# Performance work log

Hardware: AMD Instinct MI355X
Metric: run time of the kernel (lower is better)

Reference implementation:

```python
import jax, jax.numpy as jnp
import numpy as np

IN_F = 1024
OUT_F = 4096
SEARCH_SPACE = [1, 2, 4, 8, 16]  # block sizes; powers of 2 dividing both dims, capped at 16


def circ_avg(W, bs):
    """Project W [out,in] onto block-circulant structure with block size bs.

    Equivalent to trans_to_cir_meng: within each (bs x bs) block, average each
    wrap-around diagonal and rebuild a circulant block C[k, j] = c[(k - j) % bs].
    """
    q, p = W.shape[0] // bs, W.shape[1] // bs
    t = W.reshape(q, bs, p, bs).transpose(0, 2, 1, 3)  # [q, p, bs, bs]
    i = jnp.arange(bs)
    # rot[..., i, j] = t[..., i, (i + j) % bs]  (rotate rows so diagonals align in columns)
    rot = t[:, :, i[:, None], (i[:, None] + i[None, :]) % bs]  # [q, p, bs, bs]
    c = rot.mean(axis=2)  # [q, p, bs]  mean over each diagonal
    # circulant block: w[..., k, j] = c[..., (k - j) % bs]
    w = c[:, :, (i[:, None] - i[None, :]) % bs]  # [q, p, bs, bs]
    return w.transpose(0, 2, 1, 3).reshape(W.shape)


def setup_inputs() -> dict:
    key = jax.random.key(0)
    k1, k2, k3, k4 = jax.random.split(key, 4)
    x = jax.random.normal(k1, (16, 512, IN_F), dtype=jnp.float32)
    weight = jax.random.normal(k2, (OUT_F, IN_F), dtype=jnp.float32) * 0.02
    alphas = jax.random.normal(k3, (len(SEARCH_SPACE),), dtype=jnp.float32)
    bias = jax.random.normal(k4, (OUT_F,), dtype=jnp.float32) * 0.02
    return {"x": x, "weight": weight, "alphas": alphas, "bias": bias}


def reference(x, weight, alphas, bias):
    # soft NAS mixture over block sizes (tau=1, soft mode)
    a = jax.nn.softmax(alphas)
    W = a[0] * weight  # block_size 1 == original weight
    for idx, bs in enumerate(SEARCH_SPACE[1:], start=1):
        W = W + a[idx] * circ_avg(weight, bs)
    # F.linear: y = x @ W^T + b
    return jnp.einsum("bsi,oi->bso", x, W) + bias
```

## Files before the change

kernel.cpp:

```cpp
#include <hip/hip_runtime.h>

typedef __bf16 bf16;
typedef __bf16 bf16x8 __attribute__((ext_vector_type(8)));
typedef float floatx4 __attribute__((ext_vector_type(4)));

#define IN_F  1024
#define OUT_F 4096
#define M_DIM 8192
#define K_DIM 1024
#define N_DIM 4096

__device__ __forceinline__ unsigned short f2bf(float f) {
    unsigned int u = __float_as_uint(f);
    u += 0x7FFFu + ((u >> 16) & 1u);
    return (unsigned short)(u >> 16);
}

__global__ __launch_bounds__(256) void build_w_kernel(
    const float* __restrict__ W, const float* __restrict__ alphas,
    unsigned short* __restrict__ Wb)
{
    __shared__ float Wl[16 * 256];

    const int t = threadIdx.x;
    const int rb = blockIdx.x >> 2;
    const int cb = blockIdx.x & 3;
    const int row0 = rb * 16, col0 = cb * 256;

    const float4* src = (const float4*)(W + (size_t)row0 * IN_F + col0);
    #pragma unroll
    for (int j = 0; j < 4; ++j) {
        const int idx = j * 256 + t;
        const int r = idx >> 6, c4 = idx & 63;
        ((float4*)Wl)[r * 64 + c4] = src[(size_t)r * 256 + c4];
    }

    float av[5];
    float mx = -1e30f;
    #pragma unroll
    for (int j = 0; j < 5; ++j) { av[j] = alphas[j]; mx = fmaxf(mx, av[j]); }
    float s = 0.f;
    #pragma unroll
    for (int j = 0; j < 5; ++j) { av[j] = __expf(av[j] - mx); s += av[j]; }
    const float inv = 1.f / s;
    #pragma unroll
    for (int j = 0; j < 5; ++j) av[j] *= inv;

    __syncthreads();

    const int k  = t >> 4;
    const int jj = t & 15;
    unsigned short ov[16];

    #pragma unroll
    for (int jb = 0; jb < 16; ++jb) {
        const int j = jb * 16 + jj;
        float acc = av[0] * Wl[k * 256 + j];
        #pragma unroll
        for (int e = 1; e <= 4; ++e) {
            const int bs   = 1 << e;
            const int mask = bs - 1;
            const int ol = k & ~mask;
            const int il = j & ~mask;
            const int d  = (k - j) & mask;
            float ssum = 0.f;
            #pragma unroll
            for (int r = 0; r < bs; ++r)
                ssum += Wl[(ol + r) * 256 + il + ((r + d) & mask)];
            acc += av[e] * (1.0f / (float)bs) * ssum;
        }
        ov[jb] = f2bf(acc);
    }

    __syncthreads();
    unsigned short* Wls = (unsigned short*)Wl;
    #pragma unroll
    for (int jb = 0; jb < 16; ++jb)
        Wls[k * 256 + jb * 16 + jj] = ov[jb];
    __syncthreads();

    const int kr = t >> 4, cg = t & 15;
    const uint4* p = (const uint4*)(Wls + kr * 256 + cg * 16);
    uint4* dst = (uint4*)(Wb + (size_t)(row0 + kr) * IN_F + col0 + cg * 16);
    dst[0] = p[0];
    dst[1] = p[1];
}

__global__ __launch_bounds__(256) void cvt_x_kernel(
    const float* __restrict__ x, uint4* __restrict__ xb)
{
    const int t = blockIdx.x * 256 + threadIdx.x;
    const float4* xv = (const float4*)x;
    const float4 v0 = xv[2 * t];
    const float4 v1 = xv[2 * t + 1];
    uint4 o;
    o.x = (unsigned)f2bf(v0.x) | ((unsigned)f2bf(v0.y) << 16);
    o.y = (unsigned)f2bf(v0.z) | ((unsigned)f2bf(v0.w) << 16);
    o.z = (unsigned)f2bf(v1.x) | ((unsigned)f2bf(v1.y) << 16);
    o.w = (unsigned)f2bf(v1.z) | ((unsigned)f2bf(v1.w) << 16);
    xb[t] = o;
}

__global__ __launch_bounds__(256) void gemm_bt_kernel(
    const bf16* __restrict__ A, const bf16* __restrict__ B,
    const float* __restrict__ bias, float* __restrict__ C)
{
    constexpr int N = N_DIM, K = K_DIM;
    constexpr int TM = 128, TN = 128, TK = 64;

    __shared__ __align__(16) bf16 As[TM * TK];
    __shared__ __align__(16) bf16 Bs[TN * TK];

    const int t    = threadIdx.x;
    const int w    = t >> 6;
    const int l    = t & 63;
    const int quad = l >> 4;
    const int l16  = l & 15;
    const int x7   = l16 & 7;

    const int nb = N / TN;
    const int bm = blockIdx.x / nb;
    const int bn = blockIdx.x % nb;

    const int wm = (w >> 1) * 64;
    const int wn = (w & 1) * 64;

    floatx4 acc[4][4] = {};

    int crow[4], ccol[4], loff[4];
    #pragma unroll
    for (int q = 0; q < 4; ++q) {
        const int chunk = q * 256 + t;
        crow[q] = chunk >> 3;
        ccol[q] = (((chunk & 7) ^ ((chunk >> 3) & 7)) * 8);
        loff[q] = (q * 256 + (t & ~63)) * 8;
    }

    const bf16* Abase = A + (size_t)bm * TM * K;
    const bf16* Bbase = B + (size_t)bn * TN * K;

    for (int kt = 0; kt < K; kt += TK) {
        #pragma unroll
        for (int q = 0; q < 4; ++q) {
            __builtin_amdgcn_global_load_lds(
                (const __attribute__((address_space(1))) void*)(Abase + (size_t)crow[q] * K + kt + ccol[q]),
                (__attribute__((address_space(3))) void*)(As + loff[q]), 16, 0, 0);
        }
        #pragma unroll
        for (int q = 0; q < 4; ++q) {
            __builtin_amdgcn_global_load_lds(
                (const __attribute__((address_space(1))) void*)(Bbase + (size_t)crow[q] * K + kt + ccol[q]),
                (__attribute__((address_space(3))) void*)(Bs + loff[q]), 16, 0, 0);
        }
        __syncthreads();

        #pragma unroll
        for (int ks = 0; ks < 2; ++ks) {
            bf16x8 af[4], bfr[4];
            const int kx = ((ks * 4 + quad) ^ x7) * 8;
            #pragma unroll
            for (int mt = 0; mt < 4; ++mt)
                af[mt] = *(const bf16x8*)(As + (wm + mt * 16 + l16) * TK + kx);
            #pragma unroll
            for (int nt = 0; nt < 4; ++nt)
                bfr[nt] = *(const bf16x8*)(Bs + (wn + nt * 16 + l16) * TK + kx);
            #pragma unroll
            for (int mt = 0; mt < 4; ++mt)
                #pragma unroll
                for (int nt = 0; nt < 4; ++nt)
                    acc[mt][nt] = __builtin_amdgcn_mfma_f32_16x16x32_bf16(
                        af[mt], bfr[nt], acc[mt][nt], 0, 0, 0);
        }
        __syncthreads();
    }

    float bv[4];
    #pragma unroll
    for (int nt = 0; nt < 4; ++nt)
        bv[nt] = bias[bn * TN + wn + nt * 16 + l16];

    float* Cbase = C + (size_t)(bm * TM + wm) * N + bn * TN + wn;
    #pragma unroll
    for (int mt = 0; mt < 4; ++mt) {
        #pragma unroll
        for (int r = 0; r < 4; ++r) {
            float* crowp = Cbase + (size_t)(mt * 16 + quad * 4 + r) * N;
            #pragma unroll
            for (int nt = 0; nt < 4; ++nt)
                crowp[nt * 16 + l16] = acc[mt][nt][r] + bv[nt];
        }
    }
}

extern "C" void kernel_launch(void* const* d_in, const int* in_sizes, int n_in,
                              void* d_out, int out_size, void* d_ws, size_t ws_size,
                              hipStream_t stream) {
    const float* x      = (const float*)d_in[0];
    const float* weight = (const float*)d_in[1];
    const float* alphas = (const float*)d_in[2];
    const float* bias   = (const float*)d_in[3];
    float* out = (float*)d_out;

    unsigned short* Wb = (unsigned short*)d_ws;
    unsigned short* Xb = (unsigned short*)((char*)d_ws + (size_t)OUT_F * IN_F * 2);

    build_w_kernel<<<(OUT_F / 16) * (IN_F / 256), 256, 0, stream>>>(weight, alphas, Wb);
    cvt_x_kernel<<<(M_DIM * K_DIM / 8) / 256, 256, 0, stream>>>(x, (uint4*)Xb);

    const int grid = (M_DIM / 128) * (N_DIM / 128);
    gemm_bt_kernel<<<grid, 256, 0, stream>>>((const bf16*)Xb, (const bf16*)Wb, bias, out);
}
```

Measured before the change: 250.0 us.

## Enlarge GEMM tile to 256x128, load A directly to registers, rotate build_w columns

The GEMM block tile grows to 256x128. Each wave now owns 64 rows across the full 128 columns and loads its A fragments straight from global memory into registers instead of staging them in LDS, so only B is shared through LDS. This cuts LDS traffic and the LDS footprint and doubles per-wave accumulator reuse, at the cost of more registers (32 accumulators) and uncoalesced direct global loads for A. Separately, build_w_kernel rotates each thread's column order by its row index, which is meant to spread LDS bank accesses across threads.

```diff
diff --git a/kernel.cpp b/kernel.cpp
--- a/kernel.cpp
+++ b/kernel.cpp
@@ -54,7 +54,8 @@
 
     #pragma unroll
     for (int jb = 0; jb < 16; ++jb) {
-        const int j = jb * 16 + jj;
+        const int jr = (jb + k) & 15;
+        const int j  = jr * 16 + jj;
         float acc = av[0] * Wl[k * 256 + j];
         #pragma unroll
         for (int e = 1; e <= 4; ++e) {
@@ -75,8 +76,10 @@
     __syncthreads();
     unsigned short* Wls = (unsigned short*)Wl;
     #pragma unroll
-    for (int jb = 0; jb < 16; ++jb)
-        Wls[k * 256 + jb * 16 + jj] = ov[jb];
+    for (int jb = 0; jb < 16; ++jb) {
+        const int jr = (jb + k) & 15;
+        Wls[k * 256 + jr * 16 + jj] = ov[jb];
+    }
     __syncthreads();
 
     const int kr = t >> 4, cg = t & 15;
@@ -101,14 +104,13 @@
     xb[t] = o;
 }
 
-__global__ __launch_bounds__(256) void gemm_bt_kernel(
+__global__ __launch_bounds__(256, 2) void gemm_bt_kernel(
     const bf16* __restrict__ A, const bf16* __restrict__ B,
     const float* __restrict__ bias, float* __restrict__ C)
 {
     constexpr int N = N_DIM, K = K_DIM;
-    constexpr int TM = 128, TN = 128, TK = 64;
-
-    __shared__ __align__(16) bf16 As[TM * TK];
+    constexpr int TM = 256, TN = 128, TK = 64;
+
     __shared__ __align__(16) bf16 Bs[TN * TK];
 
     const int t    = threadIdx.x;
@@ -121,11 +123,9 @@
     const int nb = N / TN;
     const int bm = blockIdx.x / nb;
     const int bn = blockIdx.x % nb;
-
-    const int wm = (w >> 1) * 64;
-    const int wn = (w & 1) * 64;
-
-    floatx4 acc[4][4] = {};
+    const int wm = w * 64;
+
+    floatx4 acc[4][8] = {};
 
     int crow[4], ccol[4], loff[4];
     #pragma unroll
@@ -136,57 +136,56 @@
         loff[q] = (q * 256 + (t & ~63)) * 8;
     }
 
-    const bf16* Abase = A + (size_t)bm * TM * K;
+    const bf16* Abase = A + (size_t)(bm * TM + wm) * K;
     const bf16* Bbase = B + (size_t)bn * TN * K;
 
+    #pragma unroll 1
     for (int kt = 0; kt < K; kt += TK) {
-        #pragma unroll
-        for (int q = 0; q < 4; ++q) {
-            __builtin_amdgcn_global_load_lds(
-                (const __attribute__((address_space(1))) void*)(Abase + (size_t)crow[q] * K + kt + ccol[q]),
-                (__attribute__((address_space(3))) void*)(As + loff[q]), 16, 0, 0);
-        }
         #pragma unroll
         for (int q = 0; q < 4; ++q) {
             __builtin_amdgcn_global_load_lds(
                 (const __attribute__((address_space(1))) void*)(Bbase + (size_t)crow[q] * K + kt + ccol[q]),
                 (__attribute__((address_space(3))) void*)(Bs + loff[q]), 16, 0, 0);
         }
+        bf16x8 af[2][4];
+        #pragma unroll
+        for (int ks = 0; ks < 2; ++ks)
+            #pragma unroll
+            for (int mt = 0; mt < 4; ++mt)
+                af[ks][mt] = *(const bf16x8*)(Abase + (size_t)(mt * 16 + l16) * K
+                                              + kt + ks * 32 + quad * 8);
         __syncthreads();
 
         #pragma unroll
         for (int ks = 0; ks < 2; ++ks) {
-            bf16x8 af[4], bfr[4];
+            bf16x8 bfr[8];
             const int kx = ((ks * 4 + quad) ^ x7) * 8;
             #pragma unroll
-            for (int mt = 0; mt < 4; ++mt)
-                af[mt] = *(const bf16x8*)(As + (wm + mt * 16 + l16) * TK + kx);
-            #pragma unroll
-            for (int nt = 0; nt < 4; ++nt)
-                bfr[nt] = *(const bf16x8*)(Bs + (wn + nt * 16 + l16) * TK + kx);
+            for (int nt = 0; nt < 8; ++nt)
+                bfr[nt] = *(const bf16x8*)(Bs + (nt * 16 + l16) * TK + kx);
             #pragma unroll
             for (int mt = 0; mt < 4; ++mt)
                 #pragma unroll
-                for (int nt = 0; nt < 4; ++nt)
+                for (int nt = 0; nt < 8; ++nt)
                     acc[mt][nt] = __builtin_amdgcn_mfma_f32_16x16x32_bf16(
-                        af[mt], bfr[nt], acc[mt][nt], 0, 0, 0);
+                        af[ks][mt], bfr[nt], acc[mt][nt], 0, 0, 0);
         }
         __syncthreads();
     }
 
-    float bv[4];
-    #pragma unroll
-    for (int nt = 0; nt < 4; ++nt)
-        bv[nt] = bias[bn * TN + wn + nt * 16 + l16];
-
-    float* Cbase = C + (size_t)(bm * TM + wm) * N + bn * TN + wn;
+    float bv[8];
+    #pragma unroll
+    for (int nt = 0; nt < 8; ++nt)
+        bv[nt] = bias[bn * TN + nt * 16 + l16];
+
+    float* Cbase = C + (size_t)(bm * TM + wm) * N + bn * TN;
     #pragma unroll
     for (int mt = 0; mt < 4; ++mt) {
         #pragma unroll
         for (int r = 0; r < 4; ++r) {
             float* crowp = Cbase + (size_t)(mt * 16 + quad * 4 + r) * N;
             #pragma unroll
-            for (int nt = 0; nt < 4; ++nt)
+            for (int nt = 0; nt < 8; ++nt)
                 crowp[nt * 16 + l16] = acc[mt][nt][r] + bv[nt];
         }
     }
@@ -207,6 +206,6 @@
     build_w_kernel<<<(OUT_F / 16) * (IN_F / 256), 256, 0, stream>>>(weight, alphas, Wb);
     cvt_x_kernel<<<(M_DIM * K_DIM / 8) / 256, 256, 0, stream>>>(x, (uint4*)Xb);
 
-    const int grid = (M_DIM / 128) * (N_DIM / 128);
+    const int grid = (M_DIM / 256) * (N_DIM / 128);
     gemm_bt_kernel<<<grid, 256, 0, stream>>>((const bf16*)Xb, (const bf16*)Wb, bias, out);
 }
```

Result: no change. 251.3 us (+0.5%).
